# Kernel optimization log

Measured on AMD Instinct MI355X. Metric: run time of the kernel, lower is better.

## Reference

```python
import jax, jax.numpy as jnp
import numpy as np

CODEBOOK_SIZE = 1024
LATENT_DIM = 256
COMMITMENT_COST = 0.25
EMA_DECAY = 0.99
EPS = 1e-05


def setup_inputs() -> dict:
    key = jax.random.key(0)
    k1, k2, k3 = jax.random.split(key, 3)
    B, D, T, K = 32, LATENT_DIM, 2048, CODEBOOK_SIZE
    z = jax.random.normal(k1, (B, D, T), dtype=jnp.float32)
    embedding = jax.random.normal(k2, (K, D), dtype=jnp.float32) * (1.0 / K)
    ema_count = jnp.ones((K,), dtype=jnp.float32)
    ema_weight = jax.random.normal(k3, (K, D), dtype=jnp.float32) * (1.0 / K)
    return {"z": z, "embedding": embedding, "ema_count": ema_count, "ema_weight": ema_weight}


def reference(z, embedding, ema_count, ema_weight):
    B, D, T = z.shape
    K = embedding.shape[0]
    # (B, D, T) -> (B*T, D)
    z_flat = jnp.transpose(z, (0, 2, 1)).reshape(-1, D)

    # Squared L2 distances: ||z||^2 + ||e||^2 - 2 z.e
    d = (jnp.sum(z_flat * z_flat, axis=1, keepdims=True)
         + jnp.sum(embedding * embedding, axis=1)[None, :]
         - 2.0 * (z_flat @ embedding.T))  # (N, K)
    token_ids_flat = jnp.argmin(d, axis=1)  # (N,)
    z_q_flat = embedding[token_ids_flat]    # (N, D)

    # Losses (stop_gradient mirrors .detach())
    commitment_loss = jnp.mean((z_flat - jax.lax.stop_gradient(z_q_flat)) ** 2)
    codebook_loss = jnp.mean((z_q_flat - jax.lax.stop_gradient(z_flat)) ** 2)
    vq_loss = codebook_loss + COMMITMENT_COST * commitment_loss

    # Straight-through estimator
    z_q_flat_ste = z_flat + jax.lax.stop_gradient(z_q_flat - z_flat)
    z_q = jnp.transpose(z_q_flat_ste.reshape(B, T, D), (0, 2, 1))
    token_ids = token_ids_flat.reshape(B, T)

    # EMA codebook update (training-mode, no-grad)
    zf = jax.lax.stop_gradient(z_flat)
    ids = jax.lax.stop_gradient(token_ids_flat)
    counts = jax.ops.segment_sum(jnp.ones_like(zf[:, 0]), ids, num_segments=K)  # (K,)
    sums = jax.ops.segment_sum(zf, ids, num_segments=K)                          # (K, D)
    new_ema_count = EMA_DECAY * ema_count + (1.0 - EMA_DECAY) * counts
    new_ema_weight = EMA_DECAY * ema_weight + (1.0 - EMA_DECAY) * sums
    n = jnp.sum(new_ema_count)
    smoothed = (new_ema_count + EPS) / (n + K * EPS) * n
    new_embedding = new_ema_weight / smoothed[:, None]

    return z_q, token_ids, vq_loss, new_embedding, new_ema_count, new_ema_weight
```

## Files before the change

kernel.cpp:

```cpp
#include <hip/hip_runtime.h>
#include <hip/hip_bf16.h>
#include <string.h>

#define D_ 256
#define K_ 1024
#define T_ 2048
#define B_ 32
#define N_ 65536

#define OFF_ZQ   0u
#define OFF_IDS  16777216u
#define OFF_LOSS 16842752u
#define OFF_EMB  16842753u
#define OFF_CNT  17104897u
#define OFF_W    17105921u

#define WS_IDS     0x000000u
#define WS_ZN      0x040000u
#define WS_ORDER   0x080000u
#define WS_SUMS    0x0C0000u
#define WS_COUNTS  0x1C0000u
#define WS_EN      0x1C1000u
#define WS_SM      0x1C2000u
#define WS_OFFS    0x1C3000u
#define WS_CURSOR  0x1C4000u
#define WS_LOSS    0x1C5000u
#define WS_END_SM  0x1C6000u
#define WS_ESPLIT  0x290000u
#define WS_TOP2    0x390000u
#define WS_ZSPLIT  0x1000000u
#define WS_END_XL  0x3000000u

#define TAU 2.0e-4f

typedef float f32x4 __attribute__((ext_vector_type(4)));
typedef _Float16 f16x8 __attribute__((ext_vector_type(8)));
typedef unsigned short ushort_t;
typedef unsigned long long u64;

static __device__ inline float fmul_rn_opaque(float a, float b) {
  float r = a * b;
  asm volatile("" : "+v"(r));
  return r;
}

static __device__ inline ushort_t f2h(float x) {
  _Float16 h = (_Float16)x;
  ushort_t u;
  __builtin_memcpy(&u, &h, 2);
  return u;
}
static __device__ inline float h2f(ushort_t u) {
  _Float16 h;
  __builtin_memcpy(&h, &u, 2);
  return (float)h;
}

static __device__ inline u64 skey(float s, int j) {
  unsigned int u = __float_as_uint(s);
  u = u ^ ((unsigned int)((int)u >> 31) | 0x80000000u);
  return ((u64)u << 32) | (unsigned int)j;
}
static __device__ inline float key_s(u64 k) {
  unsigned int u = (unsigned int)(k >> 32);
  u = (u & 0x80000000u) ? (u ^ 0x80000000u) : ~u;
  return __uint_as_float(u);
}

static __device__ __forceinline__ void gload16(const void* g, void* l) {
  __builtin_amdgcn_global_load_lds(
      (const __attribute__((address_space(1))) void*)g,
      (__attribute__((address_space(3))) void*)l, 16, 0, 0);
}

template <typename F>
static __device__ inline float np_pairwise256(F term) {
  float h0 = 0.f, h1 = 0.f;
#pragma unroll
  for (int half = 0; half < 2; ++half) {
    const int base = half * 128;
    float r[8];
#pragma unroll
    for (int k = 0; k < 8; ++k) r[k] = term(base + k);
    for (int i = 8; i < 128; i += 8) {
#pragma unroll
      for (int k = 0; k < 8; ++k) r[k] += term(base + i + k);
    }
    float v = ((r[0] + r[1]) + (r[2] + r[3])) + ((r[4] + r[5]) + (r[6] + r[7]));
    if (half == 0) h0 = v; else h1 = v;
  }
  return h0 + h1;
}

__global__ __launch_bounds__(256) void k_eprep(const float* __restrict__ emb,
                                               float* __restrict__ en,
                                               ushort_t* __restrict__ esplit) {
  const int tid = threadIdx.x;
  const int j = blockIdx.x * 32 + (tid >> 3);
  const int k = tid & 7;
  const float* e = emb + (size_t)j * D_;

  float h[2];
#pragma unroll
  for (int half = 0; half < 2; ++half) {
    float r = 0.f;
    for (int i = 0; i < 16; ++i) {
      float x = e[half * 128 + 8 * i + k];
      float t = fmul_rn_opaque(x, x);
      r = (i == 0) ? t : r + t;
    }
    float s = r + __shfl_xor(r, 1, 64);
    s = s + __shfl_xor(s, 2, 64);
    s = s + __shfl_xor(s, 4, 64);
    h[half] = s;
  }
  if (k == 0) en[j] = h[0] + h[1];

  ushort_t* er = esplit + (size_t)j * 256;
#pragma unroll
  for (int m = 0; m < 32; m += 4) {
    float4 v = *reinterpret_cast<const float4*>(e + k * 32 + m);
    *reinterpret_cast<ushort4*>(er + k * 32 + m) =
        make_ushort4(f2h(v.x * 256.f), f2h(v.y * 256.f),
                     f2h(v.z * 256.f), f2h(v.w * 256.f));
  }
}

__global__ __launch_bounds__(256) void k_zprep(const float* __restrict__ z,
                                               float* __restrict__ zn,
                                               ushort_t* __restrict__ zsplit) {
  __shared__ float tile[64][68];
  const int tid = threadIdx.x, bid = blockIdx.x;
  const int tchunk = bid & 31, b = bid >> 5;
  const int n0 = b * T_ + tchunk * 64;
  const int tt = tid & 63, q = tid >> 6;
  const int tok = tid >> 2, p = tid & 3;

  float r0 = 0.f, r1 = 0.f, h0 = 0.f;
  for (int c = 0; c < 4; ++c) {
    __syncthreads();
    const float* zp = z + (size_t)b * D_ * T_ + (size_t)(c * 64) * T_ + tchunk * 64;
#pragma unroll
    for (int i = 0; i < 16; ++i) {
      int dd = q + 4 * i;
      tile[dd][tt] = zp[(size_t)dd * T_ + tt];
    }
    __syncthreads();
    {
      ushort_t* dst = zsplit + (size_t)(n0 + tok) * 256 + c * 64 + p * 16;
#pragma unroll
      for (int jj = 0; jj < 16; jj += 2) {
        float x0 = tile[p * 16 + jj][tok];
        float x1 = tile[p * 16 + jj + 1][tok];
        *reinterpret_cast<ushort2*>(dst + jj) = make_ushort2(f2h(x0), f2h(x1));
      }
    }
#pragma unroll
    for (int il = 0; il < 8; ++il) {
      float x0 = tile[8 * il + 2 * p][tok];
      float x1 = tile[8 * il + 2 * p + 1][tok];
      float t0 = fmul_rn_opaque(x0, x0);
      float t1 = fmul_rn_opaque(x1, x1);
      if ((c & 1) == 0 && il == 0) { r0 = t0; r1 = t1; }
      else { r0 += t0; r1 += t1; }
    }
    if (c & 1) {
      float s = r0 + r1;
      s = s + __shfl_xor(s, 1, 64);
      s = s + __shfl_xor(s, 2, 64);
      if (c == 1) h0 = s;
      else if (p == 0) zn[n0 + tok] = h0 + s;
    }
  }
}

static __device__ inline void top2merge(u64& k1, u64& k2, u64 o1, u64 o2) {
  if (o1 < k1) { u64 t = k1 < o2 ? k1 : o2; k2 = t; k1 = o1; }
  else { k2 = k2 < o1 ? k2 : o1; }
}

__global__ __launch_bounds__(512) void k_gemm(
    const ushort_t* __restrict__ zsplit, const ushort_t* __restrict__ esplit,
    const float* __restrict__ en, ulonglong2* __restrict__ top2) {
  __shared__ char ldsbuf[65536];

  const int tid = threadIdx.x;
  const int w = blockIdx.x;
  const int xcd = w & 7;
  const int local = w >> 3;
  const int tt = (xcd << 5) + (local >> 2);
  const int ct = local & 3;
  const int r0 = tt * 256, c0 = ct * 256;

  const int lane = tid & 63;
  const int wv = tid >> 6;
  const int wm = wv >> 2, wn = wv & 3;
  const int m16 = lane & 15;
  const int g = lane >> 4;
  const int gb = g << 4;

  const int rl = lane >> 3;
  const int vlane = rl * 512 + ((((lane & 7) << 4)) ^ (rl << 4));
  const char* gza = (const char*)zsplit + (size_t)(r0 + wv * 32) * 512 + vlane;
  const char* gea = (const char*)esplit + (size_t)(c0 + wv * 32) * 512 + vlane;

  f32x4 acc[8][4];
#pragma unroll
  for (int mi = 0; mi < 8; ++mi)
#pragma unroll
    for (int ni = 0; ni < 4; ++ni) acc[mi][ni] = f32x4{0.f, 0.f, 0.f, 0.f};

  auto STAGE = [&](int it_) {
    const int kb = it_ << 7;
    char* lz = ldsbuf + wv * 4096;
    char* le = ldsbuf + 32768 + wv * 4096;
    const char* ga = gza + kb;
    const char* ge = gea + kb;
#pragma unroll
    for (int i = 0; i < 4; ++i) {
      gload16(ga + i * 4096, lz + i * 1024);
      gload16(ge + i * 4096, le + i * 1024);
    }
  };

  STAGE(0);
  __builtin_amdgcn_sched_barrier(0);

  const char* Zb = ldsbuf;
  const char* Eb = ldsbuf + 32768;
  for (int it = 0; it < 4; ++it) {
    asm volatile("s_waitcnt vmcnt(0)" ::: "memory");
    __builtin_amdgcn_sched_barrier(0);
    __builtin_amdgcn_s_barrier();
    __builtin_amdgcn_sched_barrier(0);

#pragma unroll
    for (int ks = 0; ks < 2; ++ks) {
      f16x8 ef[8], zf[4];
#pragma unroll
      for (int mi = 0; mi < 8; ++mi) {
        int row = wm * 128 + mi * 16 + m16;
        ef[mi] = *reinterpret_cast<const f16x8*>(
            Eb + row * 128 + (((ks << 6) + gb) ^ ((row & 7) << 4)));
      }
#pragma unroll
      for (int ni = 0; ni < 4; ++ni) {
        int row = wn * 64 + ni * 16 + m16;
        zf[ni] = *reinterpret_cast<const f16x8*>(
            Zb + row * 128 + (((ks << 6) + gb) ^ ((row & 7) << 4)));
      }
#pragma unroll
      for (int mi = 0; mi < 8; ++mi)
#pragma unroll
        for (int ni = 0; ni < 4; ++ni)
          acc[mi][ni] = __builtin_amdgcn_mfma_f32_16x16x32_f16(
              ef[mi], zf[ni], acc[mi][ni], 0, 0, 0);
    }
    asm volatile("s_waitcnt lgkmcnt(0)" ::: "memory");
    __builtin_amdgcn_sched_barrier(0);
    __builtin_amdgcn_s_barrier();
    __builtin_amdgcn_sched_barrier(0);
    if (it < 3) STAGE(it + 1);
    __builtin_amdgcn_sched_barrier(0);
  }

  u64* pairbuf = (u64*)ldsbuf;
  float env[8][4];
#pragma unroll
  for (int mi = 0; mi < 8; ++mi)
#pragma unroll
    for (int rg = 0; rg < 4; ++rg)
      env[mi][rg] = en[c0 + wm * 128 + mi * 16 + g * 4 + rg];

#pragma unroll
  for (int ni = 0; ni < 4; ++ni) {
    const int tok = wn * 64 + ni * 16 + m16;
    u64 k1 = ~0ull, k2 = ~0ull;
#pragma unroll
    for (int mi = 0; mi < 8; ++mi) {
#pragma unroll
      for (int rg = 0; rg < 4; ++rg) {
        int j = c0 + wm * 128 + mi * 16 + g * 4 + rg;
        float s = env[mi][rg] - acc[mi][ni][rg] * 0.0078125f;
        u64 key = skey(s, j);
        if (key < k1) { k2 = k1; k1 = key; }
        else if (key < k2) { k2 = key; }
      }
    }
    u64 o1 = (u64)__shfl_xor((long long)k1, 16, 64);
    u64 o2 = (u64)__shfl_xor((long long)k2, 16, 64);
    top2merge(k1, k2, o1, o2);
    o1 = (u64)__shfl_xor((long long)k1, 32, 64);
    o2 = (u64)__shfl_xor((long long)k2, 32, 64);
    top2merge(k1, k2, o1, o2);
    if (g == 0) {
      pairbuf[(tok * 2 + wm) * 2 + 0] = k1;
      pairbuf[(tok * 2 + wm) * 2 + 1] = k2;
    }
  }
  __syncthreads();
  if (tid < 256) {
    u64 a1 = pairbuf[(tid * 2 + 0) * 2 + 0], a2 = pairbuf[(tid * 2 + 0) * 2 + 1];
    top2merge(a1, a2, pairbuf[(tid * 2 + 1) * 2 + 0], pairbuf[(tid * 2 + 1) * 2 + 1]);
    top2[(size_t)(r0 + tid) * 4 + ct] = make_ulonglong2(a1, a2);
  }
}

__global__ __launch_bounds__(256) void k_merge(
    const ulonglong2* __restrict__ top2, const float* __restrict__ z,
    const float* __restrict__ emb, const float* __restrict__ en,
    const float* __restrict__ zn, int* __restrict__ ids,
    float* __restrict__ counts, float* __restrict__ out) {
  int n = blockIdx.x * 256 + threadIdx.x;
  const ulonglong2* tp = top2 + (size_t)n * 4;
  u64 k[8];
#pragma unroll
  for (int i = 0; i < 4; ++i) {
    ulonglong2 v = tp[i];
    k[2 * i] = v.x; k[2 * i + 1] = v.y;
  }
  u64 mn = k[0];
#pragma unroll
  for (int i = 1; i < 8; ++i) mn = k[i] < mn ? k[i] : mn;
  float lim = key_s(mn) + TAU;
  int cnt = 0;
  int cj[4] = {0, 0, 0, 0};
#pragma unroll
  for (int i = 0; i < 8; ++i) {
    if (key_s(k[i]) <= lim) {
      if (cnt < 4) cj[cnt] = (int)(k[i] & 1023u);
      cnt++;
    }
  }
  int jf;
  if (cnt == 1) {
    jf = (int)(mn & 1023u);
  } else {
    int b = n >> 11, t = n & 2047;
    const float* zb = z + (size_t)b * (D_ * (size_t)T_) + t;
    const float* e0 = emb + (size_t)cj[0] * D_;
    const float* e1 = emb + (size_t)cj[1] * D_;
    const float* e2 = emb + (size_t)cj[2] * D_;
    const float* e3 = emb + (size_t)cj[3] * D_;
    float a0 = 0.f, a1 = 0.f, a2 = 0.f, a3 = 0.f;
    for (int d = 0; d < D_; ++d) {
      float zv = zb[(size_t)d * T_];
      a0 = fmaf(zv, e0[d], a0);
      a1 = fmaf(zv, e1[d], a1);
      a2 = fmaf(zv, e2[d], a2);
      a3 = fmaf(zv, e3[d], a3);
    }
    float zv_n = zn[n];
    float av[4] = {a0, a1, a2, a3};
    u64 best = ~0ull;
#pragma unroll
    for (int c = 0; c < 4; ++c) {
      if (c < cnt) {
        float A = zv_n + en[cj[c]];
        float s = A - 2.0f * av[c];
        u64 key = skey(s, cj[c]);
        best = key < best ? key : best;
      }
    }
    jf = (int)(best & 1023u);
  }
  ids[n] = jf;
  out[OFF_IDS + (unsigned)n] = (float)jf;
  unsafeAtomicAdd(&counts[jf], 1.0f);
}

__global__ __launch_bounds__(1024) void k_offsets(const float* __restrict__ counts,
                                                  int* __restrict__ offs,
                                                  int* __restrict__ cursor) {
  int k = threadIdx.x;
  int c = (int)counts[k];
  __shared__ int s[1024];
  s[k] = c;
  __syncthreads();
  for (int off = 1; off < 1024; off <<= 1) {
    int v = (k >= off) ? s[k - off] : 0;
    __syncthreads();
    s[k] += v;
    __syncthreads();
  }
  int excl = s[k] - c;
  offs[k] = excl;
  cursor[k] = excl;
}

__global__ __launch_bounds__(256) void k_bucket(const int* __restrict__ ids,
                                                int* __restrict__ cursor,
                                                int* __restrict__ order) {
  int n = blockIdx.x * 256 + threadIdx.x;
  int id = ids[n] & 1023;
  int slot = atomicAdd(&cursor[id], 1);
  order[slot & (N_ - 1)] = (id << 16) | n;
}

__global__ __launch_bounds__(256) void k_sums_bf(const ushort_t* __restrict__ zsplit,
                                                 const int* __restrict__ order,
                                                 float* __restrict__ sums) {
  __shared__ int pk[128];
  const int tid = threadIdx.x;
  if (tid < 128) pk[tid] = order[blockIdx.x * 128 + tid];
  __syncthreads();
  const int half = tid >> 7;
  const int l = tid & 127;
  const int s0 = half * 64;
  float a0 = 0.f, a1 = 0.f;
  int cur = pk[s0] >> 16;
#pragma unroll 4
  for (int i = 0; i < 64; ++i) {
    int v = pk[s0 + i];
    int code = v >> 16;
    if (code != cur) {
      unsafeAtomicAdd(&sums[(size_t)cur * D_ + 2 * l], a0);
      unsafeAtomicAdd(&sums[(size_t)cur * D_ + 2 * l + 1], a1);
      a0 = 0.f; a1 = 0.f; cur = code;
    }
    const char* row = (const char*)zsplit + (size_t)(v & 0xFFFF) * 512;
    unsigned int hw = *reinterpret_cast<const unsigned int*>(row + 4 * l);
    a0 += h2f((ushort_t)(hw & 0xFFFF));
    a1 += h2f((ushort_t)(hw >> 16));
  }
  unsafeAtomicAdd(&sums[(size_t)cur * D_ + 2 * l], a0);
  unsafeAtomicAdd(&sums[(size_t)cur * D_ + 2 * l + 1], a1);
}

__global__ __launch_bounds__(256) void k_zq_loss(
    const float* __restrict__ z, const float* __restrict__ emb,
    const int* __restrict__ ids, double* __restrict__ loss,
    float* __restrict__ out) {
  __shared__ float tile[64][68];
  __shared__ float ls[4];
  const int tid = threadIdx.x;
  const int bid = blockIdx.x;
  const int tchunk = bid & 31;
  const int dchunk = (bid >> 5) & 3;
  const int b = bid >> 7;
  const int n0 = b * T_ + tchunk * 64;
  {
    int tok = tid >> 2, part = tid & 3;
    int id = ids[n0 + tok] & 1023;
    const float* er = emb + (size_t)id * D_ + dchunk * 64 + part * 16;
#pragma unroll
    for (int k = 0; k < 4; ++k) {
      float4 v = *reinterpret_cast<const float4*>(er + 4 * k);
      int d = part * 16 + 4 * k;
      tile[d + 0][tok] = v.x; tile[d + 1][tok] = v.y;
      tile[d + 2][tok] = v.z; tile[d + 3][tok] = v.w;
    }
  }
  __syncthreads();
  const int t4 = tid & 15, dq = tid >> 4;
  const size_t zbase = (size_t)b * D_ * T_ + (size_t)(dchunk * 64) * T_ + tchunk * 64;
  float acc = 0.f;
#pragma unroll
  for (int i = 0; i < 4; ++i) {
    int dd = dq + 16 * i;
    size_t a = zbase + (size_t)dd * T_ + t4 * 4;
    float4 zv = *reinterpret_cast<const float4*>(z + a);
    float4 ev = *reinterpret_cast<const float4*>(&tile[dd][t4 * 4]);
    float dx = zv.x - ev.x, dy = zv.y - ev.y, dz = zv.z - ev.z, dw = zv.w - ev.w;
    acc += dx * dx + dy * dy + dz * dz + dw * dw;
    *reinterpret_cast<float4*>(out + OFF_ZQ + a) = ev;
  }
#pragma unroll
  for (int o = 32; o; o >>= 1) acc += __shfl_down(acc, o);
  if ((tid & 63) == 0) ls[tid >> 6] = acc;
  __syncthreads();
  if (tid == 0) unsafeAtomicAdd(loss, (double)(ls[0] + ls[1] + ls[2] + ls[3]));
}

__global__ __launch_bounds__(256) void k_weight(
    const float* __restrict__ ema_count, const float* __restrict__ counts,
    const float* __restrict__ ema_weight, const float* __restrict__ sums,
    const double* __restrict__ loss, float* __restrict__ out) {
  const int k = blockIdx.x;
  const int tid = threadIdx.x;
  __shared__ float red[4];

  float part = 0.f;
#pragma unroll
  for (int i = 0; i < 4; ++i) {
    int idx = tid + 256 * i;
    part += 0.99f * ema_count[idx] + 0.01f * counts[idx];
  }
#pragma unroll
  for (int o = 32; o; o >>= 1) part += __shfl_down(part, o);
  if ((tid & 63) == 0) red[tid >> 6] = part;
  __syncthreads();
  float n = red[0] + red[1] + red[2] + red[3];

  float nck = 0.99f * ema_count[k] + 0.01f * counts[k];
  float smo = (nck + 1.0e-5f) / (n + 1024.0f * 1.0e-5f) * n;

  int i = k * 256 + tid;
  float w = 0.99f * ema_weight[i] + 0.01f * sums[i];
  out[OFF_W + i] = w;
  out[OFF_EMB + i] = w / smo;
  if (tid == 0) {
    out[OFF_CNT + k] = nck;
    if (k == 0) {
      double mean = loss[0] / 16777216.0;
      out[OFF_LOSS] = (float)(1.25 * mean);
    }
  }
}

__global__ __launch_bounds__(256) void k_en(const float* __restrict__ emb,
                                            float* __restrict__ en) {
  int j = blockIdx.x * 256 + threadIdx.x;
  const float* e = emb + (size_t)j * D_;
  en[j] = np_pairwise256([&](int d) { float x = e[d]; return fmul_rn_opaque(x, x); });
}

__global__ __launch_bounds__(256) void k_zn(const float* __restrict__ z,
                                            float* __restrict__ zn) {
  int n = blockIdx.x * 256 + threadIdx.x;
  int b = n >> 11, t = n & 2047;
  const float* zp = z + (size_t)b * (D_ * (size_t)T_) + t;
  zn[n] = np_pairwise256([&](int d) {
    float x = zp[(size_t)d * T_];
    return fmul_rn_opaque(x, x);
  });
}

__global__ __launch_bounds__(256) void k_assign(
    const float* __restrict__ z, const float* __restrict__ emb,
    const float* __restrict__ en, const float* __restrict__ zn,
    int* __restrict__ ids, float* __restrict__ counts,
    float* __restrict__ out) {
  __shared__ float zs[16][128];
  __shared__ float es[16][128];
  const int tid = threadIdx.x;
  const int tx = tid & 31;
  const int ty = tid >> 5;
  const int r0 = blockIdx.x * 128;
  const int b  = r0 >> 11;
  const int t0 = r0 & 2047;
  const float* zb = z + (size_t)b * (D_ * (size_t)T_) + t0;
  u64 keys[16];
#pragma unroll
  for (int r = 0; r < 16; ++r) keys[r] = ~0ull;
  for (int jc = 0; jc < K_; jc += 128) {
    float acc[16][4];
#pragma unroll
    for (int r = 0; r < 16; ++r)
#pragma unroll
      for (int c = 0; c < 4; ++c) acc[r][c] = 0.f;
    for (int d0 = 0; d0 < D_; d0 += 16) {
      __syncthreads();
#pragma unroll
      for (int i = 0; i < 2; ++i) {
        int slot = tid + 256 * i;
        int dd = slot >> 5, t4 = slot & 31;
        *reinterpret_cast<float4*>(&zs[dd][t4 * 4]) =
            *reinterpret_cast<const float4*>(&zb[(size_t)(d0 + dd) * T_ + t4 * 4]);
      }
#pragma unroll
      for (int i = 0; i < 2; ++i) {
        int slot = tid + 256 * i;
        int c = slot & 127, g = slot >> 7;
        int dd0 = g * 4;
        float4 ev = *reinterpret_cast<const float4*>(
            &emb[(size_t)(jc + c) * D_ + d0 + dd0]);
        es[dd0 + 0][c] = ev.x; es[dd0 + 1][c] = ev.y;
        es[dd0 + 2][c] = ev.z; es[dd0 + 3][c] = ev.w;
      }
      __syncthreads();
#pragma unroll
      for (int dd = 0; dd < 16; ++dd) {
        float4 e4 = *reinterpret_cast<const float4*>(&es[dd][tx * 4]);
        float4 z0 = *reinterpret_cast<const float4*>(&zs[dd][ty * 16]);
        float4 z1 = *reinterpret_cast<const float4*>(&zs[dd][ty * 16 + 4]);
        float4 z2 = *reinterpret_cast<const float4*>(&zs[dd][ty * 16 + 8]);
        float4 z3 = *reinterpret_cast<const float4*>(&zs[dd][ty * 16 + 12]);
        float zr[16] = {z0.x, z0.y, z0.z, z0.w, z1.x, z1.y, z1.z, z1.w,
                        z2.x, z2.y, z2.z, z2.w, z3.x, z3.y, z3.z, z3.w};
        float ec[4] = {e4.x, e4.y, e4.z, e4.w};
#pragma unroll
        for (int r = 0; r < 16; ++r)
#pragma unroll
          for (int c = 0; c < 4; ++c) acc[r][c] += zr[r] * ec[c];
      }
    }
#pragma unroll
    for (int r = 0; r < 16; ++r) {
      float znp = zn[r0 + ty * 16 + r];
      u64 kk = keys[r];
#pragma unroll
      for (int c = 0; c < 4; ++c) {
        int j = jc + tx * 4 + c;
        float A = znp + en[j];
        float s = A - 2.0f * acc[r][c];
        u64 key = skey(s, j);
        kk = key < kk ? key : kk;
      }
      keys[r] = kk;
    }
  }
#pragma unroll
  for (int r = 0; r < 16; ++r) {
    u64 kk = keys[r];
#pragma unroll
    for (int m = 1; m < 32; m <<= 1) {
      u64 o = (u64)__shfl_xor((long long)kk, m, 32);
      kk = o < kk ? o : kk;
    }
    keys[r] = kk;
  }
  if ((tid & 31) == 0) {
#pragma unroll
    for (int r = 0; r < 16; ++r) {
      int n = r0 + ty * 16 + r;
      int jf = (int)(keys[r] & 1023u);
      ids[n] = jf;
      out[OFF_IDS + (unsigned)n] = (float)jf;
      unsafeAtomicAdd(&counts[jf], 1.0f);
    }
  }
}

__global__ __launch_bounds__(256) void k_scatter_atomic(
    const float* __restrict__ z, const float* __restrict__ emb,
    const int* __restrict__ ids, float* __restrict__ sums,
    double* __restrict__ loss, float* __restrict__ out) {
  const int tid = threadIdx.x;
  unsigned int gi = blockIdx.x * 256u + (unsigned int)tid;
  int t4 = (int)(gi & 511u);
  int bd = (int)(gi >> 9);
  int d  = bd & 255;
  int b  = bd >> 8;
  size_t base = (size_t)bd * T_ + (size_t)t4 * 4;
  const float4 zv = *reinterpret_cast<const float4*>(z + base);
  const int tb = b * T_ + t4 * 4;
  float zz[4] = {zv.x, zv.y, zv.z, zv.w};
  float e4[4];
  float acc = 0.f;
#pragma unroll
  for (int u = 0; u < 4; ++u) {
    int id = ids[tb + u] & 1023;
    float e = emb[(size_t)id * D_ + d];
    float df = zz[u] - e;
    acc += df * df;
    e4[u] = e;
    unsafeAtomicAdd(&sums[(size_t)id * D_ + d], zz[u]);
  }
  *reinterpret_cast<float4*>(out + OFF_ZQ + base) =
      make_float4(e4[0], e4[1], e4[2], e4[3]);
#pragma unroll
  for (int o = 32; o; o >>= 1) acc += __shfl_down(acc, o);
  __shared__ float ls[4];
  int lane = tid & 63, wid = tid >> 6;
  if (lane == 0) ls[wid] = acc;
  __syncthreads();
  if (tid == 0) unsafeAtomicAdd(loss, (double)(ls[0] + ls[1] + ls[2] + ls[3]));
}

__global__ __launch_bounds__(1024) void k_count_fb(
    const float* __restrict__ ema_count, const float* __restrict__ counts,
    float* __restrict__ sm, const double* __restrict__ loss,
    float* __restrict__ out) {
  int k = threadIdx.x;
  float nc = 0.99f * ema_count[k] + 0.01f * counts[k];
  __shared__ float red[1024];
  red[k] = nc;
  __syncthreads();
  for (int s = 512; s > 0; s >>= 1) {
    if (k < s) red[k] += red[k + s];
    __syncthreads();
  }
  float n = red[0];
  float smo = (nc + 1.0e-5f) / (n + 1024.0f * 1.0e-5f) * n;
  sm[k] = smo;
  out[OFF_CNT + k] = nc;
  if (k == 0) {
    double mean = loss[0] / 16777216.0;
    out[OFF_LOSS] = (float)(1.25 * mean);
  }
}

__global__ __launch_bounds__(256) void k_weight_fb(
    const float* __restrict__ ema_weight, const float* __restrict__ sums,
    const float* __restrict__ sm, float* __restrict__ out) {
  int i = blockIdx.x * 256 + threadIdx.x;
  int k = i >> 8;
  float w = 0.99f * ema_weight[i] + 0.01f * sums[i];
  out[OFF_W + i] = w;
  out[OFF_EMB + i] = w / sm[k];
}

extern "C" void kernel_launch(void* const* d_in, const int* in_sizes, int n_in,
                              void* d_out, int out_size, void* d_ws, size_t ws_size,
                              hipStream_t stream) {
  const float* z          = (const float*)d_in[0];
  const float* emb        = (const float*)d_in[1];
  const float* ema_count  = (const float*)d_in[2];
  const float* ema_weight = (const float*)d_in[3];
  float* out = (float*)d_out;
  char* ws = (char*)d_ws;
  if (ws_size < (size_t)WS_END_SM) return;

  int*    ids    = (int*)(ws + WS_IDS);
  float*  zn     = (float*)(ws + WS_ZN);
  int*    order  = (int*)(ws + WS_ORDER);
  float*  sums   = (float*)(ws + WS_SUMS);
  float*  counts = (float*)(ws + WS_COUNTS);
  float*  en     = (float*)(ws + WS_EN);
  float*  sm     = (float*)(ws + WS_SM);
  int*    offs   = (int*)(ws + WS_OFFS);
  int*    cursor = (int*)(ws + WS_CURSOR);
  double* loss   = (double*)(ws + WS_LOSS);

  hipMemsetAsync(ws + WS_SUMS, 0, WS_END_SM - WS_SUMS, stream);

  if (ws_size >= (size_t)WS_END_XL) {
    ushort_t*   esplit = (ushort_t*)(ws + WS_ESPLIT);
    ushort_t*   zsplit = (ushort_t*)(ws + WS_ZSPLIT);
    ulonglong2* top2   = (ulonglong2*)(ws + WS_TOP2);

    k_eprep  <<<K_ / 32, 256, 0, stream>>>(emb, en, esplit);
    k_zprep  <<<B_ * (T_ / 64), 256, 0, stream>>>(z, zn, zsplit);
    k_gemm   <<<(K_ / 256) * (N_ / 256), 512, 0, stream>>>(zsplit, esplit, en, top2);
    k_merge  <<<N_ / 256, 256, 0, stream>>>(top2, z, emb, en, zn, ids, counts, out);
    k_offsets<<<1, 1024, 0, stream>>>(counts, offs, cursor);
    k_bucket <<<N_ / 256, 256, 0, stream>>>(ids, cursor, order);
    k_sums_bf<<<N_ / 128, 256, 0, stream>>>(zsplit, order, sums);
    k_zq_loss<<<B_ * (D_ / 64) * (T_ / 64), 256, 0, stream>>>(z, emb, ids, loss, out);
    k_weight <<<K_, 256, 0, stream>>>(ema_count, counts, ema_weight, sums, loss, out);
  } else {
    k_en <<<K_ / 256, 256, 0, stream>>>(emb, en);
    k_zn <<<N_ / 256, 256, 0, stream>>>(z, zn);
    k_assign<<<N_ / 128, 256, 0, stream>>>(z, emb, en, zn, ids, counts, out);
    k_scatter_atomic<<<(N_ * (D_ / 4)) / 256, 256, 0, stream>>>(z, emb, ids, sums, loss, out);
    k_count_fb <<<1, 1024, 0, stream>>>(ema_count, counts, sm, loss, out);
    k_weight_fb<<<(K_ * D_) / 256, 256, 0, stream>>>(ema_weight, sums, sm, out);
  }
}
```

Before: 225.3 us.

## Derive VQ loss from argmin distances and vectorize z prep loads/stores

The loss is now computed in the merge kernel from the winning distance (||z||^2 + ||e||^2 - 2 z.e), so the z_q kernel no longer rereads z and only writes the gathered codebook rows. z prep also loads z with float4 reads and packs the fp16 split values into 16-byte stores. This removes a full pass over z (64 MB) but makes the loss depend on the approximate GEMM distance in the cnt==1 path. That risks precision drift from cancellation and fp16-split error.

```diff
diff --git a/kernel.cpp b/kernel.cpp
--- a/kernel.cpp
+++ b/kernel.cpp
@@ -133,7 +133,7 @@
   const int tid = threadIdx.x, bid = blockIdx.x;
   const int tchunk = bid & 31, b = bid >> 5;
   const int n0 = b * T_ + tchunk * 64;
-  const int tt = tid & 63, q = tid >> 6;
+  const int t4 = tid & 15, rq = tid >> 4;
   const int tok = tid >> 2, p = tid & 3;
 
   float r0 = 0.f, r1 = 0.f, h0 = 0.f;
@@ -141,19 +141,23 @@
     __syncthreads();
     const float* zp = z + (size_t)b * D_ * T_ + (size_t)(c * 64) * T_ + tchunk * 64;
 #pragma unroll
-    for (int i = 0; i < 16; ++i) {
-      int dd = q + 4 * i;
-      tile[dd][tt] = zp[(size_t)dd * T_ + tt];
+    for (int i = 0; i < 4; ++i) {
+      int dd = rq + 16 * i;
+      *reinterpret_cast<float4*>(&tile[dd][t4 * 4]) =
+          *reinterpret_cast<const float4*>(&zp[(size_t)dd * T_ + t4 * 4]);
     }
     __syncthreads();
     {
       ushort_t* dst = zsplit + (size_t)(n0 + tok) * 256 + c * 64 + p * 16;
+      unsigned int wbuf[8];
 #pragma unroll
       for (int jj = 0; jj < 16; jj += 2) {
         float x0 = tile[p * 16 + jj][tok];
         float x1 = tile[p * 16 + jj + 1][tok];
-        *reinterpret_cast<ushort2*>(dst + jj) = make_ushort2(f2h(x0), f2h(x1));
-      }
+        wbuf[jj >> 1] = (unsigned int)f2h(x0) | ((unsigned int)f2h(x1) << 16);
+      }
+      *reinterpret_cast<uint4*>(dst) = make_uint4(wbuf[0], wbuf[1], wbuf[2], wbuf[3]);
+      *reinterpret_cast<uint4*>(dst + 8) = make_uint4(wbuf[4], wbuf[5], wbuf[6], wbuf[7]);
     }
 #pragma unroll
     for (int il = 0; il < 8; ++il) {
@@ -310,9 +314,11 @@
     const ulonglong2* __restrict__ top2, const float* __restrict__ z,
     const float* __restrict__ emb, const float* __restrict__ en,
     const float* __restrict__ zn, int* __restrict__ ids,
-    float* __restrict__ counts, float* __restrict__ out) {
+    float* __restrict__ counts, double* __restrict__ loss,
+    float* __restrict__ out) {
   int n = blockIdx.x * 256 + threadIdx.x;
   const ulonglong2* tp = top2 + (size_t)n * 4;
+  const float znv = zn[n];
   u64 k[8];
 #pragma unroll
   for (int i = 0; i < 4; ++i) {
@@ -333,8 +339,10 @@
     }
   }
   int jf;
+  float loss_n;
   if (cnt == 1) {
     jf = (int)(mn & 1023u);
+    loss_n = znv + key_s(mn);
   } else {
     int b = n >> 11, t = n & 2047;
     const float* zb = z + (size_t)b * (D_ * (size_t)T_) + t;
@@ -350,23 +358,33 @@
       a2 = fmaf(zv, e2[d], a2);
       a3 = fmaf(zv, e3[d], a3);
     }
-    float zv_n = zn[n];
     float av[4] = {a0, a1, a2, a3};
     u64 best = ~0ull;
 #pragma unroll
     for (int c = 0; c < 4; ++c) {
       if (c < cnt) {
-        float A = zv_n + en[cj[c]];
+        float A = znv + en[cj[c]];
         float s = A - 2.0f * av[c];
         u64 key = skey(s, cj[c]);
         best = key < best ? key : best;
       }
     }
     jf = (int)(best & 1023u);
+    loss_n = key_s(best);
   }
   ids[n] = jf;
   out[OFF_IDS + (unsigned)n] = (float)jf;
   unsafeAtomicAdd(&counts[jf], 1.0f);
+
+  float acc = loss_n;
+#pragma unroll
+  for (int o = 32; o; o >>= 1) acc += __shfl_down(acc, o);
+  __shared__ float ls[4];
+  int tid = threadIdx.x;
+  if ((tid & 63) == 0) ls[tid >> 6] = acc;
+  __syncthreads();
+  if (tid == 0)
+    unsafeAtomicAdd(loss, (double)(ls[0] + ls[1] + ls[2] + ls[3]));
 }
 
 __global__ __launch_bounds__(1024) void k_offsets(const float* __restrict__ counts,
@@ -427,12 +445,10 @@
   unsafeAtomicAdd(&sums[(size_t)cur * D_ + 2 * l + 1], a1);
 }
 
-__global__ __launch_bounds__(256) void k_zq_loss(
-    const float* __restrict__ z, const float* __restrict__ emb,
-    const int* __restrict__ ids, double* __restrict__ loss,
+__global__ __launch_bounds__(256) void k_zq(
+    const float* __restrict__ emb, const int* __restrict__ ids,
     float* __restrict__ out) {
   __shared__ float tile[64][68];
-  __shared__ float ls[4];
   const int tid = threadIdx.x;
   const int bid = blockIdx.x;
   const int tchunk = bid & 31;
@@ -454,22 +470,13 @@
   __syncthreads();
   const int t4 = tid & 15, dq = tid >> 4;
   const size_t zbase = (size_t)b * D_ * T_ + (size_t)(dchunk * 64) * T_ + tchunk * 64;
-  float acc = 0.f;
 #pragma unroll
   for (int i = 0; i < 4; ++i) {
     int dd = dq + 16 * i;
     size_t a = zbase + (size_t)dd * T_ + t4 * 4;
-    float4 zv = *reinterpret_cast<const float4*>(z + a);
-    float4 ev = *reinterpret_cast<const float4*>(&tile[dd][t4 * 4]);
-    float dx = zv.x - ev.x, dy = zv.y - ev.y, dz = zv.z - ev.z, dw = zv.w - ev.w;
-    acc += dx * dx + dy * dy + dz * dz + dw * dw;
-    *reinterpret_cast<float4*>(out + OFF_ZQ + a) = ev;
-  }
-#pragma unroll
-  for (int o = 32; o; o >>= 1) acc += __shfl_down(acc, o);
-  if ((tid & 63) == 0) ls[tid >> 6] = acc;
-  __syncthreads();
-  if (tid == 0) unsafeAtomicAdd(loss, (double)(ls[0] + ls[1] + ls[2] + ls[3]));
+    *reinterpret_cast<float4*>(out + OFF_ZQ + a) =
+        *reinterpret_cast<const float4*>(&tile[dd][t4 * 4]);
+  }
 }
 
 __global__ __launch_bounds__(256) void k_weight(
@@ -723,11 +730,11 @@
     k_eprep  <<<K_ / 32, 256, 0, stream>>>(emb, en, esplit);
     k_zprep  <<<B_ * (T_ / 64), 256, 0, stream>>>(z, zn, zsplit);
     k_gemm   <<<(K_ / 256) * (N_ / 256), 512, 0, stream>>>(zsplit, esplit, en, top2);
-    k_merge  <<<N_ / 256, 256, 0, stream>>>(top2, z, emb, en, zn, ids, counts, out);
+    k_merge  <<<N_ / 256, 256, 0, stream>>>(top2, z, emb, en, zn, ids, counts, loss, out);
     k_offsets<<<1, 1024, 0, stream>>>(counts, offs, cursor);
     k_bucket <<<N_ / 256, 256, 0, stream>>>(ids, cursor, order);
     k_sums_bf<<<N_ / 128, 256, 0, stream>>>(zsplit, order, sums);
-    k_zq_loss<<<B_ * (D_ / 64) * (T_ / 64), 256, 0, stream>>>(z, emb, ids, loss, out);
+    k_zq     <<<B_ * (D_ / 64) * (T_ / 64), 256, 0, stream>>>(emb, ids, out);
     k_weight <<<K_, 256, 0, stream>>>(ema_count, counts, ema_weight, sums, loss, out);
   } else {
     k_en <<<K_ / 256, 256, 0, stream>>>(emb, en);
```

Measured after the change: 181.7 us, median of 2. -19.4%, faster.
